# Optimization experiments

Measured on AMD Instinct MI355X. Metric: run time of the kernel, lower is better.

## Reference

```python
import jax, jax.numpy as jnp
import numpy as np

NUM_TOKENS, TOKEN_DIM, NUM_HEADS, REF_DIM = 10, 96, 4, 96


def setup_inputs() -> dict:
    key = jax.random.key(0)
    k0, k1, k2, k3, k4 = jax.random.split(key, 5)
    ref_emb = jax.random.normal(k0, (32, 2048, REF_DIM), dtype=jnp.float32)
    tokens = jax.random.normal(k1, (NUM_TOKENS, TOKEN_DIM), dtype=jnp.float32)
    # nn.Linear weights are [out, in]; forward computes x @ W.T
    Wq = jax.random.normal(k2, (TOKEN_DIM, REF_DIM), dtype=jnp.float32) * (1.0 / np.sqrt(REF_DIM))
    Wk = jax.random.normal(k3, (TOKEN_DIM, TOKEN_DIM), dtype=jnp.float32) * (1.0 / np.sqrt(TOKEN_DIM))
    Wv = jax.random.normal(k4, (NUM_HEADS, TOKEN_DIM), dtype=jnp.float32) * (1.0 / np.sqrt(TOKEN_DIM))
    return {"ref_emb": ref_emb, "tokens": tokens, "Wq": Wq, "Wk": Wk, "Wv": Wv}


def reference(ref_emb, tokens, Wq, Wk, Wv):
    # k: (N, D) tanh'd projected tokens
    k = jnp.tanh(tokens @ Wk.T)
    # q: (B, T, D)
    q = jnp.tanh(ref_emb @ Wq.T)
    # additive attention scores: s (B, T, N, D)
    s = jnp.tanh(q[:, :, None, :] + k[None, None, :, :])
    # logits: (B, T, N, H)
    logits = jnp.einsum('btnd,hd->btnh', s, Wv)
    attn = jax.nn.softmax(logits, axis=2)  # softmax over tokens
    # style: (B, T, D, H) -> mean over heads -> (B, T, D)
    style = jnp.einsum('btnh,nd->btdh', attn, tokens).mean(axis=-1)
    return style
```

## Files before the change

kernel.cpp:

```cpp
#include <hip/hip_runtime.h>
#include <rocwmma/rocwmma.hpp>
#include <cstddef>

#define NT 10
#define TD 96
#define NH 4
#define NPOS (32 * 2048)
#define TPB 256
#define PPB 32
#define LDX 104

#define WS_WQ 0
#define WS_KV2 18432
#define WS_WVP 23040
#define WS_BYTES 23808

typedef _Float16 h2 __attribute__((ext_vector_type(2)));

__device__ __forceinline__ h2 pack_h2(float a, float b) {
    return __builtin_bit_cast(h2, __builtin_amdgcn_cvt_pkrtz(a, b));
}

__device__ __forceinline__ float fast_tanh(float x) {
    float e = __expf(2.0f * x);
    return 1.0f - 2.0f * __builtin_amdgcn_rcpf(e + 1.0f);
}

__device__ __forceinline__ float dot2acc(h2 a, h2 b, float c) {
#if __has_builtin(__builtin_amdgcn_fdot2)
    return __builtin_amdgcn_fdot2(a, b, c, false);
#else
    c = fmaf((float)a[0], (float)b[0], c);
    return fmaf((float)a[1], (float)b[1], c);
#endif
}

__global__ __launch_bounds__(256) void gst_prep(
    const float* __restrict__ tokens,
    const float* __restrict__ Wq,
    const float* __restrict__ Wk,
    const float* __restrict__ Wv,
    char* __restrict__ ws)
{
    h2* wqH = (h2*)(ws + WS_WQ);
    float* kv2 = (float*)(ws + WS_KV2);
    h2* wvp = (h2*)(ws + WS_WVP);
    const int b = blockIdx.x;
    const int tid = threadIdx.x;

    if (tid < 2 * (TD / 2)) {
        int r = 2 * b + tid / (TD / 2);
        int c = tid % (TD / 2);
        float2 f = ((const float2*)(Wq + r * TD))[c];
        wqH[r * (TD / 2) + c] = pack_h2(f.x, f.y);
    }
    if (tid < 2 * NT) {
        int d = 2 * b + tid / NT;
        int n = tid % NT;
        const float4* tr = (const float4*)(tokens + n * TD);
        const float4* wr = (const float4*)(Wk + d * TD);
        float acc = 0.0f;
        #pragma unroll
        for (int j = 0; j < TD / 4; ++j) {
            float4 a = tr[j];
            float4 w = wr[j];
            acc = fmaf(a.x, w.x, acc);
            acc = fmaf(a.y, w.y, acc);
            acc = fmaf(a.z, w.z, acc);
            acc = fmaf(a.w, w.w, acc);
        }
        kv2[d * 12 + n] = fast_tanh(fast_tanh(acc));
    }
    if (tid < 2 * 2) {
        int d = 2 * b + (tid >> 1);
        kv2[d * 12 + 10 + (tid & 1)] = 0.0f;
    }
    if (b == 0 && tid < 192) {
        int pp = tid >> 5;
        int l = (tid >> 2) & 7;
        int h = tid & 3;
        wvp[(pp * 8 + l) * 4 + h] =
            pack_h2(Wv[h * TD + 16 * pp + l], Wv[h * TD + 16 * pp + 8 + l]);
    }
}

__global__ __launch_bounds__(TPB, 6) void gst_main(
    const float* __restrict__ ref_emb,
    const float* __restrict__ tokens,
    const char* __restrict__ ws,
    float* __restrict__ out)
{
    __shared__ __align__(16) char buf[PPB * LDX * 2];
    __shared__ __align__(16) float tqS[PPB * LDX];

    const int tid = threadIdx.x;
    const int P0 = blockIdx.x * PPB;
    _Float16* xS = (_Float16*)buf;

    const float4* srcKV = (const float4*)(ws + WS_KV2);
    float4 rs0 = srcKV[tid];
    float4 rs1;
    if (tid < 80) rs1 = srcKV[256 + tid];

    {
        const float4* src = (const float4*)(ref_emb + (size_t)P0 * TD);
        #pragma unroll
        for (int it = 0; it < 3; ++it) {
            int t = tid + it * TPB;
            int row = t / (TD / 4);
            int c4 = t - row * (TD / 4);
            float4 v = src[t];
            h2* dst = (h2*)(xS + row * LDX + c4 * 4);
            dst[0] = pack_h2(v.x, v.y);
            dst[1] = pack_h2(v.z, v.w);
        }
    }
    __syncthreads();

    {
        using namespace rocwmma;
        const int wid = tid >> 6;
        const int ph = wid >> 1;
        const int dh = wid & 1;

        fragment<matrix_a, 16, 16, 16, float16_t, row_major> fa[6];
        #pragma unroll
        for (int kb = 0; kb < 6; ++kb)
            load_matrix_sync(fa[kb],
                (const float16_t*)(xS + ph * 16 * LDX + kb * 16), LDX);

        const float16_t* wq16 = (const float16_t*)(ws + WS_WQ);
        #pragma unroll
        for (int t = 0; t < 3; ++t) {
            fragment<accumulator, 16, 16, 16, float> fc;
            fill_fragment(fc, 0.0f);
            #pragma unroll
            for (int kb = 0; kb < 6; ++kb) {
                fragment<matrix_b, 16, 16, 16, float16_t, col_major> fb;
                load_matrix_sync(fb, wq16 + (dh * 3 + t) * 16 * TD + kb * 16, TD);
                mma_sync(fc, fa[kb], fb, fc);
            }
            #pragma unroll
            for (int e = 0; e < fc.num_elements; ++e)
                fc.x[e] = fast_tanh(fast_tanh(fc.x[e]));
            store_matrix_sync(tqS + ph * 16 * LDX + (dh * 3 + t) * 16, fc, LDX,
                              mem_row_major);
        }
    }
    __syncthreads();

    {
        float4* dstKV = (float4*)buf;
        dstKV[tid] = rs0;
        if (tid < 80) dstKV[256 + tid] = rs1;
    }
    __syncthreads();

    const float* kvS = (const float*)buf;
    const h2* wvpS = (const h2*)(buf + 4608);

    const int prow = tid >> 3;
    const int pos = P0 + prow;
    const int l = tid & 7;
    const float* tqrow = tqS + prow * LDX;

    float logits[NT][NH];
    #pragma unroll
    for (int n = 0; n < NT; ++n)
        #pragma unroll
        for (int h = 0; h < NH; ++h) logits[n][h] = 0.0f;

    #pragma unroll
    for (int pp = 0; pp < 6; ++pp) {
        const int d1 = 16 * pp + l;
        const float t1 = tqrow[d1];
        const float t2 = tqrow[d1 + 8];

        const float* r1 = kvS + d1 * 12;
        const float* r2 = kvS + (d1 + 8) * 12;
        const float4 ka1 = *(const float4*)(r1);
        const float4 kb1 = *(const float4*)(r1 + 4);
        const float2 kc1 = *(const float2*)(r1 + 8);
        const float4 ka2 = *(const float4*)(r2);
        const float4 kb2 = *(const float4*)(r2 + 4);
        const float2 kc2 = *(const float2*)(r2 + 8);
        const float kv1[NT] = {ka1.x, ka1.y, ka1.z, ka1.w, kb1.x, kb1.y, kb1.z, kb1.w, kc1.x, kc1.y};
        const float kv2[NT] = {ka2.x, ka2.y, ka2.z, ka2.w, kb2.x, kb2.y, kb2.z, kb2.w, kc2.x, kc2.y};

        const h2* wrow = &wvpS[(pp * 8 + l) * 4];
        const h2 w0 = wrow[0], w1 = wrow[1], w2 = wrow[2], w3 = wrow[3];

        #pragma unroll
        for (int n = 0; n < NT; ++n) {
            float s1 = (t1 + kv1[n]) * __builtin_amdgcn_rcpf(fmaf(t1, kv1[n], 1.0f));
            float s2 = (t2 + kv2[n]) * __builtin_amdgcn_rcpf(fmaf(t2, kv2[n], 1.0f));
            h2 sp = pack_h2(s1, s2);
            logits[n][0] = dot2acc(sp, w0, logits[n][0]);
            logits[n][1] = dot2acc(sp, w1, logits[n][1]);
            logits[n][2] = dot2acc(sp, w2, logits[n][2]);
            logits[n][3] = dot2acc(sp, w3, logits[n][3]);
        }
    }

    const bool myb0 = (l & 1) != 0;
    const bool myb1 = (l & 2) != 0;
    float lh[NT];
    #pragma unroll
    for (int n = 0; n < NT; ++n) {
        float L0 = logits[n][0], L1 = logits[n][1];
        float L2 = logits[n][2], L3 = logits[n][3];
        L0 += __shfl_xor(L0, 4);
        L1 += __shfl_xor(L1, 4);
        L2 += __shfl_xor(L2, 4);
        L3 += __shfl_xor(L3, 4);
        float m0 = myb1 ? L2 : L0, m1 = myb1 ? L3 : L1;
        float t0 = myb1 ? L0 : L2, t1 = myb1 ? L1 : L3;
        m0 += __shfl_xor(t0, 2);
        m1 += __shfl_xor(t1, 2);
        float mm = myb0 ? m1 : m0, tt = myb0 ? m0 : m1;
        lh[n] = mm + __shfl_xor(tt, 1);
    }

    float m = lh[0];
    #pragma unroll
    for (int n = 1; n < NT; ++n) m = fmaxf(m, lh[n]);
    float e[NT];
    float ssum = 0.0f;
    #pragma unroll
    for (int n = 0; n < NT; ++n) {
        e[n] = __expf(lh[n] - m);
        ssum += e[n];
    }
    const float inv = 0.25f * __builtin_amdgcn_rcpf(ssum);
    float wn[NT];
    #pragma unroll
    for (int n = 0; n < NT; ++n) {
        float v = e[n] * inv;
        v += __shfl_xor(v, 1);
        v += __shfl_xor(v, 2);
        wn[n] = v;
    }

    float4* ob = (float4*)(out + (size_t)pos * TD);
    const float4* t4 = (const float4*)tokens;
    #pragma unroll
    for (int jj = 0; jj < 3; ++jj) {
        const int d4 = l + 8 * jj;
        float4 o = make_float4(0.f, 0.f, 0.f, 0.f);
        #pragma unroll
        for (int n = 0; n < NT; ++n) {
            float4 t = t4[n * (TD / 4) + d4];
            o.x = fmaf(wn[n], t.x, o.x);
            o.y = fmaf(wn[n], t.y, o.y);
            o.z = fmaf(wn[n], t.z, o.z);
            o.w = fmaf(wn[n], t.w, o.w);
        }
        ob[d4] = o;
    }
}

extern "C" void kernel_launch(void* const* d_in, const int* in_sizes, int n_in,
                              void* d_out, int out_size, void* d_ws, size_t ws_size,
                              hipStream_t stream) {
    const float* ref_emb = (const float*)d_in[0];
    const float* tokens  = (const float*)d_in[1];
    const float* Wq      = (const float*)d_in[2];
    const float* Wk      = (const float*)d_in[3];
    const float* Wv      = (const float*)d_in[4];
    float* out = (float*)d_out;

    gst_prep<<<48, 256, 0, stream>>>(tokens, Wq, Wk, Wv, (char*)d_ws);
    gst_main<<<NPOS / PPB, TPB, 0, stream>>>(ref_emb, tokens,
                                             (const char*)d_ws, out);
}
```

Before: 40.11 us.

## Rewrite tanh-of-sum as exponential product form to drop a multiply in inner loop

New measurement: 38.85 us. 3.1% less time.

```diff
diff --git a/kernel.cpp b/kernel.cpp
--- a/kernel.cpp
+++ b/kernel.cpp
@@ -8,12 +8,13 @@
 #define NPOS (32 * 2048)
 #define TPB 256
 #define PPB 32
-#define LDX 104
+#define LDQ 104
 
 #define WS_WQ 0
 #define WS_KV2 18432
 #define WS_WVP 23040
-#define WS_BYTES 23808
+#define WS_C 23808
+#define WS_BYTES 23824
 
 typedef _Float16 h2 __attribute__((ext_vector_type(2)));
 
@@ -45,6 +46,7 @@
     h2* wqH = (h2*)(ws + WS_WQ);
     float* kv2 = (float*)(ws + WS_KV2);
     h2* wvp = (h2*)(ws + WS_WVP);
+    float* Cws = (float*)(ws + WS_C);
     const int b = blockIdx.x;
     const int tid = threadIdx.x;
 
@@ -69,7 +71,7 @@
             acc = fmaf(a.z, w.z, acc);
             acc = fmaf(a.w, w.w, acc);
         }
-        kv2[d * 12 + n] = fast_tanh(fast_tanh(acc));
+        kv2[d * 12 + n] = __expf(2.0f * fast_tanh(acc));
     }
     if (tid < 2 * 2) {
         int d = 2 * b + (tid >> 1);
@@ -82,6 +84,12 @@
         wvp[(pp * 8 + l) * 4 + h] =
             pack_h2(Wv[h * TD + 16 * pp + l], Wv[h * TD + 16 * pp + 8 + l]);
     }
+    if (b == 0 && tid >= 224 && tid < 224 + NH) {
+        int h = tid - 224;
+        float c = 0.0f;
+        for (int d = 0; d < TD; ++d) c += Wv[h * TD + d];
+        Cws[h] = c;
+    }
 }
 
 __global__ __launch_bounds__(TPB, 6) void gst_main(
@@ -90,17 +98,13 @@
     const char* __restrict__ ws,
     float* __restrict__ out)
 {
-    __shared__ __align__(16) char buf[PPB * LDX * 2];
-    __shared__ __align__(16) float tqS[PPB * LDX];
+    __shared__ __align__(16) _Float16 xS[PPB * LDQ];
+    __shared__ __align__(16) _Float16 eqS[PPB * LDQ];
+    __shared__ __align__(16) float kvS[TD * 12];
+    __shared__ __align__(16) h2 wvpS[6 * 8 * 4];
 
     const int tid = threadIdx.x;
     const int P0 = blockIdx.x * PPB;
-    _Float16* xS = (_Float16*)buf;
-
-    const float4* srcKV = (const float4*)(ws + WS_KV2);
-    float4 rs0 = srcKV[tid];
-    float4 rs1;
-    if (tid < 80) rs1 = srcKV[256 + tid];
 
     {
         const float4* src = (const float4*)(ref_emb + (size_t)P0 * TD);
@@ -110,71 +114,75 @@
             int row = t / (TD / 4);
             int c4 = t - row * (TD / 4);
             float4 v = src[t];
-            h2* dst = (h2*)(xS + row * LDX + c4 * 4);
+            h2* dst = (h2*)(xS + row * LDQ + c4 * 4);
             dst[0] = pack_h2(v.x, v.y);
             dst[1] = pack_h2(v.z, v.w);
         }
+        const float4* sKV = (const float4*)(ws + WS_KV2);
+        float4* dKV = (float4*)kvS;
+        dKV[tid % 288] = sKV[tid % 288];
+        if (tid < 32) dKV[256 + tid] = sKV[256 + tid];
+        const float4* sWV = (const float4*)(ws + WS_WVP);
+        float4* dWV = (float4*)wvpS;
+        if (tid >= 64 && tid < 112) dWV[tid - 64] = sWV[tid - 64];
     }
     __syncthreads();
 
     {
         using namespace rocwmma;
+        const int lane = tid & 63;
         const int wid = tid >> 6;
         const int ph = wid >> 1;
         const int dh = wid & 1;
+        const int arow = lane & 15;
+        const int kgrp = lane >> 4;
 
         fragment<matrix_a, 16, 16, 16, float16_t, row_major> fa[6];
         #pragma unroll
         for (int kb = 0; kb < 6; ++kb)
             load_matrix_sync(fa[kb],
-                (const float16_t*)(xS + ph * 16 * LDX + kb * 16), LDX);
+                (const float16_t*)(xS + ph * 16 * LDQ + kb * 16), LDQ);
 
         const float16_t* wq16 = (const float16_t*)(ws + WS_WQ);
+        fragment<accumulator, 16, 16, 16, float> fc[3];
         #pragma unroll
         for (int t = 0; t < 3; ++t) {
-            fragment<accumulator, 16, 16, 16, float> fc;
-            fill_fragment(fc, 0.0f);
+            fill_fragment(fc[t], 0.0f);
             #pragma unroll
             for (int kb = 0; kb < 6; ++kb) {
                 fragment<matrix_b, 16, 16, 16, float16_t, col_major> fb;
                 load_matrix_sync(fb, wq16 + (dh * 3 + t) * 16 * TD + kb * 16, TD);
-                mma_sync(fc, fa[kb], fb, fc);
+                mma_sync(fc[t], fa[kb], fb, fc[t]);
             }
+        }
+        #pragma unroll
+        for (int t = 0; t < 3; ++t) {
+            const int d = dh * 48 + t * 16 + arow;
             #pragma unroll
-            for (int e = 0; e < fc.num_elements; ++e)
-                fc.x[e] = fast_tanh(fast_tanh(fc.x[e]));
-            store_matrix_sync(tqS + ph * 16 * LDX + (dh * 3 + t) * 16, fc, LDX,
-                              mem_row_major);
+            for (int e = 0; e < 4; ++e) {
+                const int p = ph * 16 + kgrp * 4 + e;
+                eqS[p * LDQ + d] = (_Float16)__expf(2.0f * fast_tanh(fc[t].x[e]));
+            }
         }
     }
     __syncthreads();
-
-    {
-        float4* dstKV = (float4*)buf;
-        dstKV[tid] = rs0;
-        if (tid < 80) dstKV[256 + tid] = rs1;
-    }
-    __syncthreads();
-
-    const float* kvS = (const float*)buf;
-    const h2* wvpS = (const h2*)(buf + 4608);
 
     const int prow = tid >> 3;
     const int pos = P0 + prow;
     const int l = tid & 7;
-    const float* tqrow = tqS + prow * LDX;
-
-    float logits[NT][NH];
+    const _Float16* eqrow = eqS + prow * LDQ;
+
+    float R[NT][NH];
     #pragma unroll
     for (int n = 0; n < NT; ++n)
         #pragma unroll
-        for (int h = 0; h < NH; ++h) logits[n][h] = 0.0f;
+        for (int h = 0; h < NH; ++h) R[n][h] = 0.0f;
 
     #pragma unroll
     for (int pp = 0; pp < 6; ++pp) {
         const int d1 = 16 * pp + l;
-        const float t1 = tqrow[d1];
-        const float t2 = tqrow[d1 + 8];
+        const float Eq1 = (float)eqrow[d1];
+        const float Eq2 = (float)eqrow[d1 + 8];
 
         const float* r1 = kvS + d1 * 12;
         const float* r2 = kvS + (d1 + 8) * 12;
@@ -184,21 +192,21 @@
         const float4 ka2 = *(const float4*)(r2);
         const float4 kb2 = *(const float4*)(r2 + 4);
         const float2 kc2 = *(const float2*)(r2 + 8);
-        const float kv1[NT] = {ka1.x, ka1.y, ka1.z, ka1.w, kb1.x, kb1.y, kb1.z, kb1.w, kc1.x, kc1.y};
-        const float kv2[NT] = {ka2.x, ka2.y, ka2.z, ka2.w, kb2.x, kb2.y, kb2.z, kb2.w, kc2.x, kc2.y};
+        const float ek1[NT] = {ka1.x, ka1.y, ka1.z, ka1.w, kb1.x, kb1.y, kb1.z, kb1.w, kc1.x, kc1.y};
+        const float ek2[NT] = {ka2.x, ka2.y, ka2.z, ka2.w, kb2.x, kb2.y, kb2.z, kb2.w, kc2.x, kc2.y};
 
         const h2* wrow = &wvpS[(pp * 8 + l) * 4];
         const h2 w0 = wrow[0], w1 = wrow[1], w2 = wrow[2], w3 = wrow[3];
 
         #pragma unroll
         for (int n = 0; n < NT; ++n) {
-            float s1 = (t1 + kv1[n]) * __builtin_amdgcn_rcpf(fmaf(t1, kv1[n], 1.0f));
-            float s2 = (t2 + kv2[n]) * __builtin_amdgcn_rcpf(fmaf(t2, kv2[n], 1.0f));
-            h2 sp = pack_h2(s1, s2);
-            logits[n][0] = dot2acc(sp, w0, logits[n][0]);
-            logits[n][1] = dot2acc(sp, w1, logits[n][1]);
-            logits[n][2] = dot2acc(sp, w2, logits[n][2]);
-            logits[n][3] = dot2acc(sp, w3, logits[n][3]);
+            float v1 = __builtin_amdgcn_rcpf(fmaf(Eq1, ek1[n], 1.0f));
+            float v2 = __builtin_amdgcn_rcpf(fmaf(Eq2, ek2[n], 1.0f));
+            h2 rp = pack_h2(v1, v2);
+            R[n][0] = dot2acc(rp, w0, R[n][0]);
+            R[n][1] = dot2acc(rp, w1, R[n][1]);
+            R[n][2] = dot2acc(rp, w2, R[n][2]);
+            R[n][3] = dot2acc(rp, w3, R[n][3]);
         }
     }
 
@@ -207,8 +215,8 @@
     float lh[NT];
     #pragma unroll
     for (int n = 0; n < NT; ++n) {
-        float L0 = logits[n][0], L1 = logits[n][1];
-        float L2 = logits[n][2], L3 = logits[n][3];
+        float L0 = R[n][0], L1 = R[n][1];
+        float L2 = R[n][2], L3 = R[n][3];
         L0 += __shfl_xor(L0, 4);
         L1 += __shfl_xor(L1, 4);
         L2 += __shfl_xor(L2, 4);
@@ -221,6 +229,14 @@
         lh[n] = mm + __shfl_xor(tt, 1);
     }
 
+    {
+        const float4 Call = *(const float4*)(ws + WS_C);
+        const float Ch = myb0 ? (myb1 ? Call.w : Call.y)
+                              : (myb1 ? Call.z : Call.x);
+        #pragma unroll
+        for (int n = 0; n < NT; ++n) lh[n] = fmaf(-2.0f, lh[n], Ch);
+    }
+
     float m = lh[0];
     #pragma unroll
     for (int n = 1; n < NT; ++n) m = fmaxf(m, lh[n]);
```
